# Performance work log

Measured on AMD Instinct MI355X. Metric: run time of the kernel, lower is better.

The kernel has to match this reference:

```python
import jax, jax.numpy as jnp
import numpy as np

B, C, H, W = 8, 384, 32, 32
NH, DK, DV = 8, 48, 48
CFF = 4 * C
L = H * W
NBIAS = (2 * H - 1) * (2 * W - 1)
LN_EPS = 1e-5


def _relative_indices(height, width):
    # rel_idx[q, k] = (gy_k - gy_q + H) * W + (gx_k - gx_q + W), matching the torch loop
    gy, gx = np.meshgrid(np.arange(height), np.arange(width), indexing='ij')
    gy = gy.ravel(); gx = gx.ravel()
    rel = (gy[None, :] - gy[:, None] + height) * width + (gx[None, :] - gx[:, None] + width)
    return jnp.asarray(rel, dtype=jnp.int64)


def setup_inputs() -> dict:
    key = jax.random.key(0)
    ks = jax.random.split(key, 10)
    s = 0.02  # small init scale
    return {
        'x': jax.random.normal(ks[0], (B, C, H, W), dtype=jnp.float32),
        'gamma': jnp.ones((C,), jnp.float32),
        'beta': jnp.zeros((C,), jnp.float32),
        'Wq': jax.random.normal(ks[1], (NH * DK, C), jnp.float32) * s,
        'Wk': jax.random.normal(ks[2], (NH * DK, C), jnp.float32) * s,
        'Wv': jax.random.normal(ks[3], (NH * DV, C), jnp.float32) * s,
        'Wo': jax.random.normal(ks[4], (C, NH * DV), jnp.float32) * s,
        'bo': jnp.zeros((C,), jnp.float32),
        'rel_bias': jax.random.normal(ks[5], (NH, NBIAS), jnp.float32),
        'fc1_w': jax.random.normal(ks[6], (CFF, C), jnp.float32) * s,
        'fc1_b': jnp.zeros((CFF,), jnp.float32),
        'fc2_w': jax.random.normal(ks[7], (C, CFF), jnp.float32) * s,
        'fc2_b': jnp.zeros((C,), jnp.float32),
        'rel_idx': _relative_indices(H, W),
    }


def reference(x, gamma, beta, Wq, Wk, Wv, Wo, bo, rel_bias,
              fc1_w, fc1_b, fc2_w, fc2_b, rel_idx):
    b, c, h_sp, w_sp = x.shape
    l = h_sp * w_sp
    nh = rel_bias.shape[0]
    dk = Wq.shape[0] // nh
    dv = Wv.shape[0] // nh

    # LayerNorm over channel dim (NHWC), then flatten to tokens [b, l, c]
    t = jnp.transpose(x, (0, 2, 3, 1))
    mu = jnp.mean(t, axis=-1, keepdims=True)
    var = jnp.mean(jnp.square(t - mu), axis=-1, keepdims=True)
    t = (t - mu) / jnp.sqrt(var + LN_EPS) * gamma + beta
    tok = t.reshape(b, l, c)

    q = (tok @ Wq.T).reshape(b, l, nh, dk)
    k = (tok @ Wk.T).reshape(b, l, nh, dk)
    v = (tok @ Wv.T).reshape(b, l, nh, dv)

    # gathered relative position bias: [nh, l, l]
    bias = rel_bias[:, rel_idx]
    # note: original applies NO 1/sqrt(d_k) scaling
    scores = jnp.einsum('blhd,bmhd->bhlm', q, k) + bias[None]
    attn = jax.nn.softmax(scores, axis=-1)
    out = jnp.einsum('bhlm,bmhd->blhd', attn, v).reshape(b, l, nh * dv)
    out = out @ Wo.T + bo  # [b, l, c]
    out = jnp.transpose(out, (0, 2, 1)).reshape(b, c, h_sp, w_sp)

    y = x + out  # attention residual (x_stem = x, no downsampling)

    # FFN: 1x1 convs == per-pixel linear over channels; exact (erf) gelu as torch default
    u = jnp.einsum('bchw,oc->bohw', y, fc1_w) + fc1_b[None, :, None, None]
    u = jax.nn.gelu(u, approximate=False)
    u = jnp.einsum('bchw,oc->bohw', u, fc2_w) + fc2_b[None, :, None, None]
    return y + u
```

## Files before the change

### kernel.cpp

```cpp
#include <hip/hip_runtime.h>
#include <math.h>

#define SL 1024
#define CH 384
#define NHEAD 8
#define DH 48
#define NBIAS 3969
#define NTOK 8192
#define BATCH 8
#define CFF 1536
#define LN_EPS 1e-5f
#define QKVLD 1152
#define HMS 3145728
#define LOG2E 1.4426950408889634f

#define WQKV_OFF 0
#define WO_OFF   442368
#define F1_OFF   589824
#define F2_OFF   1179648
#define WTOT     1769472

typedef float floatx4 __attribute__((ext_vector_type(4)));
typedef short bf16x8 __attribute__((ext_vector_type(8)));

__device__ __forceinline__ unsigned f2bf_u(float f) {
  unsigned u = __float_as_uint(f);
  return (u + 0x7fffu + ((u >> 16) & 1u)) >> 16;
}
__device__ __forceinline__ unsigned pack2(float a, float b) {
  return f2bf_u(a) | (f2bf_u(b) << 16);
}
__device__ __forceinline__ unsigned cvtpk(float lo, float hi) {
  unsigned r;
  asm("v_cvt_pk_bf16_f32 %0, %1, %2" : "=v"(r) : "v"(lo), "v"(hi));
  return r;
}

__device__ __forceinline__ void gload_lds16(const void* g, void* l) {
  __builtin_amdgcn_global_load_lds(
      (const __attribute__((address_space(1))) void*)g,
      (__attribute__((address_space(3))) void*)l, 16, 0, 0);
}

__global__ void k_w2bf(const float* __restrict__ Wq, const float* __restrict__ Wk,
                       const float* __restrict__ Wv, const float* __restrict__ Wo,
                       const float* __restrict__ f1, const float* __restrict__ f2,
                       short* __restrict__ dst) {
  size_t i = ((size_t)blockIdx.x * 256 + threadIdx.x) * 8;
  if (i >= WTOT) return;
  const float* s;
  size_t base;
  if (i < 147456)        { s = Wq; base = 0; }
  else if (i < 294912)   { s = Wk; base = 147456; }
  else if (i < WO_OFF)   { s = Wv; base = 294912; }
  else if (i < F1_OFF)   { s = Wo; base = WO_OFF; }
  else if (i < F2_OFF)   { s = f1; base = F1_OFF; }
  else                   { s = f2; base = F2_OFF; }
  const float4* p = (const float4*)(s + (i - base));
  float4 a = p[0], b = p[1];
  uint4 o;
  o.x = pack2(a.x, a.y); o.y = pack2(a.z, a.w);
  o.z = pack2(b.x, b.y); o.w = pack2(b.z, b.w);
  *(uint4*)(dst + i) = o;
}

__global__ __launch_bounds__(256) void k_ln_fused(
    const float* __restrict__ x, const float* __restrict__ gamma,
    const float* __restrict__ beta, short* __restrict__ tok) {
  __shared__ float sx[32][385];
  int b = blockIdx.y, l0 = blockIdx.x * 32;
  int tid = threadIdx.x;
  const float* xb = x + (size_t)b * CH * SL;
  int cr = tid >> 3, ls = (tid & 7) * 4;
#pragma unroll
  for (int c0 = 0; c0 < CH; c0 += 32) {
    int c = c0 + cr;
    float4 v = *(const float4*)(xb + (size_t)c * SL + l0 + ls);
    sx[ls + 0][c] = v.x; sx[ls + 1][c] = v.y;
    sx[ls + 2][c] = v.z; sx[ls + 3][c] = v.w;
  }
  __syncthreads();
  int tl = tid >> 3, p = tid & 7;
  float vals[48];
  float s = 0.f, q = 0.f;
#pragma unroll
  for (int i = 0; i < 48; i++) {
    float v = sx[tl][p * 48 + i];
    vals[i] = v; s += v; q += v * v;
  }
  s += __shfl_xor(s, 1, 64); q += __shfl_xor(q, 1, 64);
  s += __shfl_xor(s, 2, 64); q += __shfl_xor(q, 2, 64);
  s += __shfl_xor(s, 4, 64); q += __shfl_xor(q, 4, 64);
  float mu = s * (1.0f / CH);
  float rstd = rsqrtf(q * (1.0f / CH) - mu * mu + LN_EPS);
  short* orow = tok + (size_t)(b * SL + l0 + tl) * CH + p * 48;
#pragma unroll
  for (int i = 0; i < 48; i += 2) {
    float a = (vals[i] - mu) * rstd * gamma[p * 48 + i] + beta[p * 48 + i];
    float c = (vals[i + 1] - mu) * rstd * gamma[p * 48 + i + 1] + beta[p * 48 + i + 1];
    *(unsigned*)(orow + i) = pack2(a, c);
  }
}

template <int BM, bool GELU, bool HAS_BIAS, int RES_MODE, int OUT_MODE>
__global__ __launch_bounds__(256) void k_gemm_mfma(
    const short* __restrict__ A, const short* __restrict__ W,
    const float* __restrict__ bias, const float* __restrict__ res,
    float* __restrict__ Cf, short* __restrict__ Cb, float* __restrict__ Ct,
    short* __restrict__ Chm, int N, int K) {
  constexpr int MI = BM / 32;
  constexpr int ASI = BM * 2 / 64;
  __shared__ short As[BM * 64];
  __shared__ short Bs[128 * 64];
  int tid = threadIdx.x;
  int wid = tid >> 6, lane = tid & 63;
  int lanelo = lane & 15, quad = lane >> 4;
  int wm = wid & 1, wn = wid >> 1;

  int nbx = (int)gridDim.x;
  int lin = (int)blockIdx.y * nbx + (int)blockIdx.x;
  int chunk = (nbx * (int)gridDim.y) >> 3;
  int wk = (lin & 7) * chunk + (lin >> 3);
  int m0 = (wk / nbx) * BM, n0 = (wk % nbx) * 128;

  const short* Aga[ASI];
  short* Ala[ASI];
#pragma unroll
  for (int s = 0; s < ASI; s++) {
    int p = wid * (BM * 2) + s * 64 + lane;
    int row = p >> 3, ch = (p & 7) ^ (row & 7);
    Aga[s] = A + (size_t)(m0 + row) * K + ch * 8;
    Ala[s] = As + (wid * (BM * 2) + s * 64) * 8;
  }
  const short* Bga[4];
  short* Bla[4];
#pragma unroll
  for (int s = 0; s < 4; s++) {
    int p = wid * 256 + s * 64 + lane;
    int row = p >> 3, ch = (p & 7) ^ (row & 7);
    Bga[s] = W + (size_t)(n0 + row) * K + ch * 8;
    Bla[s] = Bs + (wid * 256 + s * 64) * 8;
  }

  floatx4 acc[MI][4];
#pragma unroll
  for (int i = 0; i < MI; i++)
#pragma unroll
    for (int j = 0; j < 4; j++) acc[i][j] = {0.f, 0.f, 0.f, 0.f};

  int x8 = lanelo & 7;
  int ca0 = (quad ^ x8) * 8;
  int ca1 = ((quad + 4) ^ x8) * 8;

  for (int k0 = 0; k0 < K; k0 += 64) {
    __syncthreads();
#pragma unroll
    for (int s = 0; s < ASI; s++) gload_lds16(Aga[s] + k0, Ala[s]);
#pragma unroll
    for (int s = 0; s < 4; s++) gload_lds16(Bga[s] + k0, Bla[s]);
    __syncthreads();
#pragma unroll
    for (int h = 0; h < 2; h++) {
      int co = h ? ca1 : ca0;
      bf16x8 af[MI], bq[4];
#pragma unroll
      for (int i = 0; i < MI; i++)
        af[i] = *(const bf16x8*)&As[(wm * (BM / 2) + i * 16 + lanelo) * 64 + co];
#pragma unroll
      for (int j = 0; j < 4; j++)
        bq[j] = *(const bf16x8*)&Bs[(wn * 64 + j * 16 + lanelo) * 64 + co];
#pragma unroll
      for (int i = 0; i < MI; i++)
#pragma unroll
        for (int j = 0; j < 4; j++)
          acc[i][j] = __builtin_amdgcn_mfma_f32_16x16x32_bf16(af[i], bq[j], acc[i][j], 0, 0, 0);
    }
  }

  int colb = n0 + wn * 64 + lanelo;
  float bvv[4];
#pragma unroll
  for (int j = 0; j < 4; j++) bvv[j] = HAS_BIAS ? bias[colb + j * 16] : 0.0f;
#pragma unroll
  for (int i = 0; i < MI; i++) {
    int r = m0 + wm * (BM / 2) + i * 16 + quad * 4;
    int bb = r >> 10, ll = r & 1023;
#pragma unroll
    for (int j = 0; j < 4; j++) {
      int c = colb + j * 16;
      float4 rv = {0.f, 0.f, 0.f, 0.f};
      if (RES_MODE == 2) rv = *(const float4*)(res + ((size_t)bb * CH + c) * SL + ll);
      float vv[4];
#pragma unroll
      for (int reg = 0; reg < 4; reg++) {
        float v = acc[i][j][reg] + bvv[j];
        if (RES_MODE == 1) v += res[(size_t)(r + reg) * N + c];
        if (RES_MODE == 2) v += (&rv.x)[reg];
        if (GELU) {
          float t = v * fmaf(v * v, 0.0356774081f, 0.7978845608f);
          float e = __builtin_amdgcn_exp2f(t * -2.8853900817779268f);
          v = v * __builtin_amdgcn_rcpf(e + 1.0f);
        }
        vv[reg] = v;
      }
      if (OUT_MODE & 1) {
#pragma unroll
        for (int reg = 0; reg < 4; reg++) Cf[(size_t)(r + reg) * N + c] = vv[reg];
      }
      if (OUT_MODE & 2) {
#pragma unroll
        for (int reg = 0; reg < 4; reg++) Cb[(size_t)(r + reg) * N + c] = (short)f2bf_u(vv[reg]);
      }
      if (OUT_MODE & 4) {
        float4 ov = {vv[0], vv[1], vv[2], vv[3]};
        *(float4*)(Ct + ((size_t)bb * CH + c) * SL + ll) = ov;
      }
      if (OUT_MODE & 8) {
        int part = c / 384;
        int rem = c - part * 384;
        int hh = rem / 48, dd = rem - hh * 48;
        short* dst = Chm + (size_t)part * HMS +
                     ((size_t)(bb * NHEAD + hh) * SL + ll) * 48 + dd;
#pragma unroll
        for (int reg = 0; reg < 4; reg++) dst[reg * 48] = (short)f2bf_u(vv[reg]);
      }
    }
  }
}

__global__ __launch_bounds__(256) void k_attn_mfma(
    const short* __restrict__ qh, const short* __restrict__ kh,
    const short* __restrict__ vh, const float* __restrict__ rel_bias,
    short* __restrict__ ao) {
  __shared__ short QP[128 * 72];
  __shared__ short Ks[2][64 * 72];
  __shared__ short Vts[2][48 * 72];
  float* Bb = (float*)QP;

  int lin = ((int)blockIdx.z * 8 + (int)blockIdx.y) * 8 + (int)blockIdx.x;
  int wk = (lin & 7) * 64 + (lin >> 3);
  int b = wk >> 6, h = (wk >> 3) & 7;
  int l0 = (wk & 7) * 128;
  int tid = threadIdx.x;
  int wid = tid >> 6, lane = tid & 63;
  int lanelo = lane & 15, quad = lane >> 4;
  size_t hb = ((size_t)b * NHEAD + h) * SL;
  size_t bSL = (size_t)b * SL;
  const short* kbase = kh + hb * 48;
  const short* vbase = vh + hb * 48;

  {
    const short* qsrc = qh + (hb + l0) * 48;
#pragma unroll
    for (int s = 0; s < 3; s++) {
      int g = tid + 256 * s;
      int row = g / 6, pos = g - row * 6;
      *(uint4*)&QP[row * 72 + pos * 8] = *(const uint4*)(qsrc + g * 8);
    }
  }
  for (int z = tid; z < 128 * 8; z += 256) {
    int r = z >> 3, u = z & 7;
    ((unsigned*)&QP[r * 72 + 48])[u] = 0u;
    if (r < 64) {
      ((unsigned*)&Ks[0][r * 72 + 48])[u] = 0u;
      ((unsigned*)&Ks[1][r * 72 + 48])[u] = 0u;
    }
  }
  __syncthreads();

  bf16x8 aq[2][2];
#pragma unroll
  for (int qi = 0; qi < 2; qi++) {
    aq[qi][0] = *(const bf16x8*)&QP[(wid * 32 + qi * 16 + lanelo) * 72 + quad * 8];
    aq[qi][1] = *(const bf16x8*)&QP[(wid * 32 + qi * 16 + lanelo) * 72 + 32 + quad * 8];
  }
  __syncthreads();

  int kg = 2 * tid;
  int krow = kg / 6, kpos = kg - krow * 6;
  int vmp = tid & 31, vdg = tid >> 5;
  int kk = 2 * vmp;
  int vcol = (kk & 3) + ((kk >> 2) & 3) * 8 + ((kk >> 4) & 1) * 4 + (kk >> 5) * 32;
  unsigned sel_e = 0x05040100u, sel_o = 0x07060302u;

  {
    const float* bsrc = rel_bias + h * NBIAS + (929 - l0);
    for (int j = tid; j < 1152; j += 256) Bb[j] = bsrc[j] * LOG2E;
  }
  if (tid < 192) {
    const short* ksrc = kbase + kg * 8;
    uint4 k0 = *(const uint4*)(ksrc);
    uint4 k1 = *(const uint4*)(ksrc + 8);
    const short* vs = vbase + (size_t)kk * 48 + vdg * 8;
    uint4 va = *(const uint4*)vs;
    uint4 vb = *(const uint4*)(vs + 48);
    *(uint4*)&Ks[0][krow * 72 + kpos * 8] = k0;
    *(uint4*)&Ks[0][krow * 72 + (kpos + 1) * 8] = k1;
#pragma unroll
    for (int j = 0; j < 4; j++) {
      unsigned wa = ((const unsigned*)&va)[j], wb = ((const unsigned*)&vb)[j];
      unsigned pe, po;
      asm("v_perm_b32 %0, %1, %2, %3" : "=v"(pe) : "v"(wb), "v"(wa), "v"(sel_e));
      asm("v_perm_b32 %0, %1, %2, %3" : "=v"(po) : "v"(wb), "v"(wa), "v"(sel_o));
      *(unsigned*)&Vts[0][(vdg * 8 + 2 * j + 0) * 72 + vcol] = pe;
      *(unsigned*)&Vts[0][(vdg * 8 + 2 * j + 1) * 72 + vcol] = po;
    }
  }
  __syncthreads();

  floatx4 O[3][2];
#pragma unroll
  for (int dt = 0; dt < 3; dt++)
#pragma unroll
    for (int qi = 0; qi < 2; qi++) O[dt][qi] = {0.f, 0.f, 0.f, 0.f};
  float lsum[2] = {0.f, 0.f};
  int boff[2];
#pragma unroll
  for (int qi = 0; qi < 2; qi++)
    boff[qi] = 127 + quad * 4 - (wid * 32 + qi * 16 + lanelo);

  int cur = 0;
  for (int mt = 0; mt < SL; mt += 64) {
    bool last = (mt + 64 >= SL);
    uint4 k0n, k1n, van, vbn;
    if (tid < 192 && !last) {
      int mtn = mt + 64;
      const short* ksrc = kbase + (size_t)mtn * 48 + kg * 8;
      k0n = *(const uint4*)(ksrc);
      k1n = *(const uint4*)(ksrc + 8);
      const short* vs = vbase + (size_t)(mtn + kk) * 48 + vdg * 8;
      van = *(const uint4*)vs;
      vbn = *(const uint4*)(vs + 48);
    }

    bf16x8 kb[4][2];
#pragma unroll
    for (int nt = 0; nt < 4; nt++) {
      kb[nt][0] = *(const bf16x8*)&Ks[cur][(nt * 16 + lanelo) * 72 + quad * 8];
      kb[nt][1] = *(const bf16x8*)&Ks[cur][(nt * 16 + lanelo) * 72 + 32 + quad * 8];
    }
    bf16x8 vf[3][2];
#pragma unroll
    for (int dt = 0; dt < 3; dt++) {
      vf[dt][0] = *(const bf16x8*)&Vts[cur][(dt * 16 + lanelo) * 72 + quad * 8];
      vf[dt][1] = *(const bf16x8*)&Vts[cur][(dt * 16 + lanelo) * 72 + 32 + quad * 8];
    }

#pragma unroll
    for (int qi = 0; qi < 2; qi++) {
      floatx4 sc[4];
#pragma unroll
      for (int nt = 0; nt < 4; nt++) {
        floatx4 a = {0.f, 0.f, 0.f, 0.f};
        a = __builtin_amdgcn_mfma_f32_16x16x32_bf16(kb[nt][0], aq[qi][0], a, 0, 0, 0);
        a = __builtin_amdgcn_mfma_f32_16x16x32_bf16(kb[nt][1], aq[qi][1], a, 0, 0, 0);
        sc[nt] = a;
      }
      union U8 { unsigned u[4]; bf16x8 v; };
      U8 pb0, pb1;
#pragma unroll
      for (int nt = 0; nt < 4; nt++) {
        int bidx = boff[qi] + mt + nt * 16;
        float e0 = __builtin_amdgcn_exp2f(fmaf(sc[nt][0], LOG2E, Bb[bidx + 0]));
        float e1 = __builtin_amdgcn_exp2f(fmaf(sc[nt][1], LOG2E, Bb[bidx + 1]));
        float e2 = __builtin_amdgcn_exp2f(fmaf(sc[nt][2], LOG2E, Bb[bidx + 2]));
        float e3 = __builtin_amdgcn_exp2f(fmaf(sc[nt][3], LOG2E, Bb[bidx + 3]));
        lsum[qi] += (e0 + e1) + (e2 + e3);
        unsigned p01 = cvtpk(e0, e1), p23 = cvtpk(e2, e3);
        if (nt == 0) { pb0.u[0] = p01; pb0.u[1] = p23; }
        else if (nt == 1) { pb0.u[2] = p01; pb0.u[3] = p23; }
        else if (nt == 2) { pb1.u[0] = p01; pb1.u[1] = p23; }
        else { pb1.u[2] = p01; pb1.u[3] = p23; }
      }
#pragma unroll
      for (int dt = 0; dt < 3; dt++) {
        O[dt][qi] = __builtin_amdgcn_mfma_f32_16x16x32_bf16(vf[dt][0], pb0.v, O[dt][qi], 0, 0, 0);
        O[dt][qi] = __builtin_amdgcn_mfma_f32_16x16x32_bf16(vf[dt][1], pb1.v, O[dt][qi], 0, 0, 0);
      }
    }

    if (tid < 192 && !last) {
      int nxt = cur ^ 1;
      *(uint4*)&Ks[nxt][krow * 72 + kpos * 8] = k0n;
      *(uint4*)&Ks[nxt][krow * 72 + (kpos + 1) * 8] = k1n;
#pragma unroll
      for (int j = 0; j < 4; j++) {
        unsigned wa = ((const unsigned*)&van)[j], wb = ((const unsigned*)&vbn)[j];
        unsigned pe, po;
        asm("v_perm_b32 %0, %1, %2, %3" : "=v"(pe) : "v"(wb), "v"(wa), "v"(sel_e));
        asm("v_perm_b32 %0, %1, %2, %3" : "=v"(po) : "v"(wb), "v"(wa), "v"(sel_o));
        *(unsigned*)&Vts[nxt][(vdg * 8 + 2 * j + 0) * 72 + vcol] = pe;
        *(unsigned*)&Vts[nxt][(vdg * 8 + 2 * j + 1) * 72 + vcol] = po;
      }
    }
    __syncthreads();
    cur ^= 1;
  }

  __syncthreads();
  float inv[2];
#pragma unroll
  for (int qi = 0; qi < 2; qi++) {
    float s = lsum[qi];
    s += __shfl_xor(s, 16, 64);
    s += __shfl_xor(s, 32, 64);
    inv[qi] = __builtin_amdgcn_rcpf(s);
  }
#pragma unroll
  for (int dt = 0; dt < 3; dt++)
#pragma unroll
    for (int qi = 0; qi < 2; qi++) {
      unsigned w0 = cvtpk(O[dt][qi][0] * inv[qi], O[dt][qi][1] * inv[qi]);
      unsigned w1 = cvtpk(O[dt][qi][2] * inv[qi], O[dt][qi][3] * inv[qi]);
      uint2 wv = {w0, w1};
      *(uint2*)&QP[(wid * 32 + qi * 16 + lanelo) * 72 + dt * 16 + quad * 4] = wv;
    }
  __asm__ volatile("s_waitcnt lgkmcnt(0)" ::: "memory");
#pragma unroll
  for (int s = 0; s < 3; s++) {
    int g = lane + 64 * s;
    int qloc = g / 6, pos = g - qloc * 6;
    uint4 val = *(const uint4*)&QP[(wid * 32 + qloc) * 72 + pos * 8];
    *(uint4*)(ao + (bSL + (size_t)(l0 + wid * 32 + qloc)) * CH + h * DH + pos * 8) = val;
  }
}

extern "C" void kernel_launch(void* const* d_in, const int* in_sizes, int n_in,
                              void* d_out, int out_size, void* d_ws, size_t ws_size,
                              hipStream_t stream) {
  const float* x = (const float*)d_in[0];
  const float* gamma = (const float*)d_in[1];
  const float* beta = (const float*)d_in[2];
  const float* Wq = (const float*)d_in[3];
  const float* Wk = (const float*)d_in[4];
  const float* Wv = (const float*)d_in[5];
  const float* Wo = (const float*)d_in[6];
  const float* bo = (const float*)d_in[7];
  const float* rel_bias = (const float*)d_in[8];
  const float* fc1_w = (const float*)d_in[9];
  const float* fc1_b = (const float*)d_in[10];
  const float* fc2_w = (const float*)d_in[11];
  const float* fc2_b = (const float*)d_in[12];
  float* out = (float*)d_out;

  const size_t TOKCH = (size_t)NTOK * CH;
  float* ws_f = (float*)d_ws;
  float* yb = ws_f;
  short* wbf    = (short*)(yb + TOKCH);
  short* tok_bf = wbf + WTOT;
  short* hm     = tok_bf + TOKCH;
  short* ao_bf  = hm + 3 * (size_t)HMS;
  short* yb_bf  = ao_bf + TOKCH;
  short* h1_bf  = yb_bf + TOKCH;

  k_w2bf<<<WTOT / 8 / 256, 256, 0, stream>>>(Wq, Wk, Wv, Wo, fc1_w, fc2_w, wbf);
  k_ln_fused<<<dim3(SL / 32, BATCH), 256, 0, stream>>>(x, gamma, beta, tok_bf);

  k_gemm_mfma<128, false, false, 0, 8>
      <<<dim3(QKVLD / 128, NTOK / 128), 256, 0, stream>>>(
          tok_bf, wbf + WQKV_OFF, nullptr, nullptr, nullptr, nullptr, nullptr,
          hm, QKVLD, CH);

  k_attn_mfma<<<dim3(SL / 128, NHEAD, BATCH), 256, 0, stream>>>(
      hm, hm + HMS, hm + 2 * (size_t)HMS, rel_bias, ao_bf);

  k_gemm_mfma<64, false, true, 2, 3>
      <<<dim3(CH / 128, NTOK / 64), 256, 0, stream>>>(
          ao_bf, wbf + WO_OFF, bo, x, yb, yb_bf, nullptr, nullptr, CH, CH);

  k_gemm_mfma<128, true, true, 0, 2>
      <<<dim3(CFF / 128, NTOK / 128), 256, 0, stream>>>(
          yb_bf, wbf + F1_OFF, fc1_b, nullptr, nullptr, h1_bf, nullptr, nullptr,
          CFF, CH);

  k_gemm_mfma<64, false, true, 1, 4>
      <<<dim3(CH / 128, NTOK / 64), 256, 0, stream>>>(
          h1_bf, wbf + F2_OFF, fc2_b, yb, nullptr, nullptr, out, nullptr, CH, CFF);
}
```

Baseline: 191.5 us.

## Replace LDS-staged GEMM tiles with direct global-to-register MFMA fragment loads

The GEMM kernel no longer stages A and W tiles through shared memory with global_load_lds and barriers. Each lane now loads its bf16x8 MFMA fragments straight from global memory, and K is a compile-time template parameter so the loop can be unrolled. This removes the LDS traffic and the __syncthreads stalls, but gives up the data reuse across waves that shared memory provided. Every wave now re-reads its A and B fragments through the caches with strided 16-byte accesses, which may raise L2 traffic.

```diff
diff --git a/kernel.cpp b/kernel.cpp
--- a/kernel.cpp
+++ b/kernel.cpp
@@ -34,12 +34,6 @@
   unsigned r;
   asm("v_cvt_pk_bf16_f32 %0, %1, %2" : "=v"(r) : "v"(lo), "v"(hi));
   return r;
-}
-
-__device__ __forceinline__ void gload_lds16(const void* g, void* l) {
-  __builtin_amdgcn_global_load_lds(
-      (const __attribute__((address_space(1))) void*)g,
-      (__attribute__((address_space(3))) void*)l, 16, 0, 0);
 }
 
 __global__ void k_w2bf(const float* __restrict__ Wq, const float* __restrict__ Wk,
@@ -102,16 +96,13 @@
   }
 }
 
-template <int BM, bool GELU, bool HAS_BIAS, int RES_MODE, int OUT_MODE>
-__global__ __launch_bounds__(256) void k_gemm_mfma(
+template <int BM, int KT, bool GELU, bool HAS_BIAS, int RES_MODE, int OUT_MODE>
+__global__ __launch_bounds__(256) void k_gemm_dir(
     const short* __restrict__ A, const short* __restrict__ W,
     const float* __restrict__ bias, const float* __restrict__ res,
     float* __restrict__ Cf, short* __restrict__ Cb, float* __restrict__ Ct,
-    short* __restrict__ Chm, int N, int K) {
+    short* __restrict__ Chm, int N) {
   constexpr int MI = BM / 32;
-  constexpr int ASI = BM * 2 / 64;
-  __shared__ short As[BM * 64];
-  __shared__ short Bs[128 * 64];
   int tid = threadIdx.x;
   int wid = tid >> 6, lane = tid & 63;
   int lanelo = lane & 15, quad = lane >> 4;
@@ -123,24 +114,14 @@
   int wk = (lin & 7) * chunk + (lin >> 3);
   int m0 = (wk / nbx) * BM, n0 = (wk % nbx) * 128;
 
-  const short* Aga[ASI];
-  short* Ala[ASI];
-#pragma unroll
-  for (int s = 0; s < ASI; s++) {
-    int p = wid * (BM * 2) + s * 64 + lane;
-    int row = p >> 3, ch = (p & 7) ^ (row & 7);
-    Aga[s] = A + (size_t)(m0 + row) * K + ch * 8;
-    Ala[s] = As + (wid * (BM * 2) + s * 64) * 8;
-  }
-  const short* Bga[4];
-  short* Bla[4];
-#pragma unroll
-  for (int s = 0; s < 4; s++) {
-    int p = wid * 256 + s * 64 + lane;
-    int row = p >> 3, ch = (p & 7) ^ (row & 7);
-    Bga[s] = W + (size_t)(n0 + row) * K + ch * 8;
-    Bla[s] = Bs + (wid * 256 + s * 64) * 8;
-  }
+  const short* ap[MI];
+  const short* bp[4];
+#pragma unroll
+  for (int i = 0; i < MI; i++)
+    ap[i] = A + (size_t)(m0 + wm * (BM / 2) + i * 16 + lanelo) * KT + quad * 8;
+#pragma unroll
+  for (int j = 0; j < 4; j++)
+    bp[j] = W + (size_t)(n0 + wn * 64 + j * 16 + lanelo) * KT + quad * 8;
 
   floatx4 acc[MI][4];
 #pragma unroll
@@ -148,33 +129,18 @@
 #pragma unroll
     for (int j = 0; j < 4; j++) acc[i][j] = {0.f, 0.f, 0.f, 0.f};
 
-  int x8 = lanelo & 7;
-  int ca0 = (quad ^ x8) * 8;
-  int ca1 = ((quad + 4) ^ x8) * 8;
-
-  for (int k0 = 0; k0 < K; k0 += 64) {
-    __syncthreads();
-#pragma unroll
-    for (int s = 0; s < ASI; s++) gload_lds16(Aga[s] + k0, Ala[s]);
-#pragma unroll
-    for (int s = 0; s < 4; s++) gload_lds16(Bga[s] + k0, Bla[s]);
-    __syncthreads();
-#pragma unroll
-    for (int h = 0; h < 2; h++) {
-      int co = h ? ca1 : ca0;
-      bf16x8 af[MI], bq[4];
-#pragma unroll
-      for (int i = 0; i < MI; i++)
-        af[i] = *(const bf16x8*)&As[(wm * (BM / 2) + i * 16 + lanelo) * 64 + co];
+#pragma unroll 12
+  for (int ks = 0; ks < KT / 32; ks++) {
+    bf16x8 af[MI], bq[4];
+#pragma unroll
+    for (int i = 0; i < MI; i++) af[i] = *(const bf16x8*)(ap[i] + ks * 32);
+#pragma unroll
+    for (int j = 0; j < 4; j++) bq[j] = *(const bf16x8*)(bp[j] + ks * 32);
+#pragma unroll
+    for (int i = 0; i < MI; i++)
 #pragma unroll
       for (int j = 0; j < 4; j++)
-        bq[j] = *(const bf16x8*)&Bs[(wn * 64 + j * 16 + lanelo) * 64 + co];
-#pragma unroll
-      for (int i = 0; i < MI; i++)
-#pragma unroll
-        for (int j = 0; j < 4; j++)
-          acc[i][j] = __builtin_amdgcn_mfma_f32_16x16x32_bf16(af[i], bq[j], acc[i][j], 0, 0, 0);
-    }
+        acc[i][j] = __builtin_amdgcn_mfma_f32_16x16x32_bf16(af[i], bq[j], acc[i][j], 0, 0, 0);
   }
 
   int colb = n0 + wn * 64 + lanelo;
@@ -456,24 +422,24 @@
   k_w2bf<<<WTOT / 8 / 256, 256, 0, stream>>>(Wq, Wk, Wv, Wo, fc1_w, fc2_w, wbf);
   k_ln_fused<<<dim3(SL / 32, BATCH), 256, 0, stream>>>(x, gamma, beta, tok_bf);
 
-  k_gemm_mfma<128, false, false, 0, 8>
+  k_gemm_dir<128, 384, false, false, 0, 8>
       <<<dim3(QKVLD / 128, NTOK / 128), 256, 0, stream>>>(
           tok_bf, wbf + WQKV_OFF, nullptr, nullptr, nullptr, nullptr, nullptr,
-          hm, QKVLD, CH);
+          hm, QKVLD);
 
   k_attn_mfma<<<dim3(SL / 128, NHEAD, BATCH), 256, 0, stream>>>(
       hm, hm + HMS, hm + 2 * (size_t)HMS, rel_bias, ao_bf);
 
-  k_gemm_mfma<64, false, true, 2, 3>
+  k_gemm_dir<64, 384, false, true, 2, 3>
       <<<dim3(CH / 128, NTOK / 64), 256, 0, stream>>>(
-          ao_bf, wbf + WO_OFF, bo, x, yb, yb_bf, nullptr, nullptr, CH, CH);
-
-  k_gemm_mfma<128, true, true, 0, 2>
+          ao_bf, wbf + WO_OFF, bo, x, yb, yb_bf, nullptr, nullptr, CH);
+
+  k_gemm_dir<128, 384, true, true, 0, 2>
       <<<dim3(CFF / 128, NTOK / 128), 256, 0, stream>>>(
           yb_bf, wbf + F1_OFF, fc1_b, nullptr, nullptr, h1_bf, nullptr, nullptr,
-          CFF, CH);
-
-  k_gemm_mfma<64, false, true, 1, 4>
+          CFF);
+
+  k_gemm_dir<64, 1536, false, true, 1, 4>
       <<<dim3(CH / 128, NTOK / 64), 256, 0, stream>>>(
-          h1_bf, wbf + F2_OFF, fc2_b, yb, nullptr, nullptr, out, nullptr, CH, CFF);
-}
+          h1_bf, wbf + F2_OFF, fc2_b, yb, nullptr, nullptr, out, nullptr, CH);
+}
```

Result: slower. 290.6 us (+51.8%).
